# Kernel tuning notes

Measured on AMD Instinct MI355X. Metric: run time of the kernel, lower is better.

## Reference

```python
import jax, jax.numpy as jnp
import numpy as np

N = 50000       # nodes
E = 800000      # edges (before self loops)
F_IN = 256      # num_features
HID = 64        # hidden_dim
HEADS = 4       # num_heads
NEG = 0.2       # negative_slope
LN_EPS = 1e-5


def setup_inputs() -> dict:
    key = jax.random.key(0)
    ks = jax.random.split(key, 24)
    g = lambda k, shape, s=0.05: jax.random.normal(k, shape, jnp.float32) * s
    inp = {
        "x": jax.random.normal(ks[0], (N, F_IN), jnp.float32),
        "edge_index": jax.random.randint(ks[1], (2, E), 0, N, jnp.int32),
        # gat1: in=F_IN, out=HID per head, HEADS heads, concat=True
        "W1": g(ks[2], (HEADS * HID, F_IN)),
        "att_src1": g(ks[3], (HEADS, HID)),
        "att_dst1": g(ks[4], (HEADS, HID)),
        "b1": g(ks[5], (HEADS * HID,)),
        # gat2: in=HEADS*HID, out=HID, 1 head
        "W2": g(ks[6], (HID, HEADS * HID)),
        "att_src2": g(ks[7], (1, HID)),
        "att_dst2": g(ks[8], (1, HID)),
        "b2": g(ks[9], (HID,)),
        # lin_in residual projection
        "lin_w": g(ks[10], (HID, F_IN)),
        "lin_b": g(ks[11], (HID,)),
        # LayerNorm
        "gamma": jnp.ones((HID,), jnp.float32),
        "beta": jnp.zeros((HID,), jnp.float32),
        # GRU (1 layer, input=HID, hidden=HID), gate order r,z,n as in torch
        "w_ih": g(ks[12], (3 * HID, HID)),
        "w_hh": g(ks[13], (3 * HID, HID)),
        "b_ih": g(ks[14], (3 * HID,)),
        "b_hh": g(ks[15], (3 * HID,)),
        # fc head -> 3 classes
        "fc_w": g(ks[16], (3, HID)),
        "fc_b": g(ks[17], (3,)),
    }
    return inp


def gat_conv(x, W, att_src, att_dst, bias, src, dst, heads, n_nodes):
    """PyG-style GATConv (eval mode: no dropout). src/dst include self loops."""
    h = (x @ W.T).reshape(n_nodes, heads, -1)            # [N,H,C]
    a_src = jnp.einsum('nhc,hc->nh', h, att_src)          # [N,H]
    a_dst = jnp.einsum('nhc,hc->nh', h, att_dst)
    e = jax.nn.leaky_relu(a_src[src] + a_dst[dst], NEG)   # [E',H]
    m = jax.ops.segment_max(e, dst, num_segments=n_nodes) # scatter-softmax over dst
    e = jnp.exp(e - m[dst])
    s = jax.ops.segment_sum(e, dst, num_segments=n_nodes)
    alpha = e / s[dst]                                    # [E',H]
    out = jax.ops.segment_sum(alpha[:, :, None] * h[src], dst, num_segments=n_nodes)
    return out.reshape(n_nodes, -1) + bias                # concat heads + bias


def reference(x, edge_index, W1, att_src1, att_dst1, b1, W2, att_src2, att_dst2, b2,
              lin_w, lin_b, gamma, beta, w_ih, w_hh, b_ih, b_hh, fc_w, fc_b):
    n = x.shape[0]
    loops = jnp.arange(n, dtype=edge_index.dtype)
    src = jnp.concatenate([edge_index[0], loops])  # add_self_loops=True default
    dst = jnp.concatenate([edge_index[1], loops])

    h = jax.nn.leaky_relu(gat_conv(x, W1, att_src1, att_dst1, b1, src, dst, HEADS, n), NEG)
    # F.dropout is identity in eval mode
    h = gat_conv(h, W2, att_src2, att_dst2, b2, src, dst, 1, n)
    h = jax.nn.leaky_relu(h, NEG)
    # LayerNorm (torch uses biased variance)
    mu = h.mean(-1, keepdims=True)
    var = ((h - mu) ** 2).mean(-1, keepdims=True)
    h = (h - mu) / jnp.sqrt(var + LN_EPS) * gamma + beta
    h = h + x @ lin_w.T + lin_b
    # single-step GRU with h0 = 0 (seq_len == 1)
    gi = h @ w_ih.T + b_ih                 # [N,3C]
    i_r, i_z, i_n = jnp.split(gi, 3, axis=-1)
    h_r, h_z, h_n = jnp.split(b_hh, 3)     # W_hh @ 0 == 0
    r = jax.nn.sigmoid(i_r + h_r)
    z = jax.nn.sigmoid(i_z + h_z)
    ng = jnp.tanh(i_n + r * h_n)
    hy = (1.0 - z) * ng                    # + z * h_prev(=0)
    return hy @ fc_w.T + fc_b              # [N,3]
```

## Files before the change

kernel.cpp:

```cpp
#include <hip/hip_runtime.h>
#include <hip/hip_bf16.h>

#define N_NODES 50000
#define N_EDGES 800000
#define F_IN 256
#define HID 64
#define HEADS 4
#define NEG 0.2f
#define LN_EPS 1e-5f

typedef _Float16 half8 __attribute__((ext_vector_type(8)));
typedef _Float16 half4v __attribute__((ext_vector_type(4)));
typedef _Float16 half2v __attribute__((ext_vector_type(2)));
typedef float floatx4 __attribute__((ext_vector_type(4)));

union H2U { unsigned u; half2v h; };
union H8U { half8 v; half2v h2[4]; };

__device__ __forceinline__ float wave_sum(float v) {
    #pragma unroll
    for (int o = 32; o > 0; o >>= 1) v += __shfl_xor(v, o, 64);
    return v;
}
__device__ __forceinline__ float leaky(float x) { return x > 0.0f ? x : NEG * x; }

__device__ __forceinline__ half8 load_a8(const _Float16* p) { return *(const half8*)p; }
__device__ __forceinline__ half8 load_a8(const float* p) {
    float4 f0 = *(const float4*)p;
    float4 f1 = *(const float4*)(p + 4);
    half8 h;
    h[0] = (_Float16)f0.x; h[1] = (_Float16)f0.y;
    h[2] = (_Float16)f0.z; h[3] = (_Float16)f0.w;
    h[4] = (_Float16)f1.x; h[5] = (_Float16)f1.y;
    h[6] = (_Float16)f1.z; h[7] = (_Float16)f1.w;
    return h;
}

__global__ __launch_bounds__(256, 2)
void front_kernel(const float* __restrict__ x,
                  const float* __restrict__ W1, const float* __restrict__ lin_w,
                  const float* __restrict__ lin_b,
                  const float* __restrict__ att_s, const float* __restrict__ att_d,
                  _Float16* __restrict__ h1L, float* __restrict__ a_srcO,
                  float* __restrict__ a_dstO,
                  const int* __restrict__ src, const int* __restrict__ dst,
                  int* __restrict__ deg, int* __restrict__ colb,
                  const float* __restrict__ W2, const float* __restrict__ w_ih,
                  _Float16* __restrict__ W2h, _Float16* __restrict__ w_ihh,
                  int M, int E, int Etot, int GB, int SB) {
    if ((int)blockIdx.x >= GB) {
        int b2 = blockIdx.x - GB;
        if (b2 < SB) {
            int e = b2 * 256 + threadIdx.x;
            if (e >= Etot) return;
            int s, d;
            if (e < E) { s = src[e]; d = dst[e]; }
            else       { s = d = e - E; }
            int pos = atomicAdd(&deg[d], 1);
            if (pos < 64) colb[d * 64 + pos] = s;
        } else {
            int rel = ((b2 - SB) * 256 + threadIdx.x) * 4;
            const float* s; _Float16* dp;
            if      (rel < 16384) { s = W2; dp = W2h; }
            else if ((rel -= 16384) < 12288) { s = w_ih; dp = w_ihh; }
            else return;
            float4 v = *(const float4*)(s + rel);
            half4v h;
            h[0] = (_Float16)v.x; h[1] = (_Float16)v.y;
            h[2] = (_Float16)v.z; h[3] = (_Float16)v.w;
            *(half4v*)(dp + rel) = h;
        }
        return;
    }
    constexpr int NT = 20, Nc = 320, K = 256;
    constexpr int BROW = 40;
    constexpr int BTILE = Nc * BROW * 2;
    constexpr int NCS = 328;
    constexpr int TILE2B = 8 * NCS * 2;
    __shared__ __align__(16) char smem[BTILE];
    _Float16* sB = (_Float16*)smem;
    int tid = threadIdx.x;
    int w = tid >> 6, lane = tid & 63;
    int m_base = blockIdx.x * 64 + w * 16;
    bool active = (m_base < M);
    int r = lane & 15, q = lane >> 4;
    const float* ap = x + (size_t)(m_base + r) * K + q * 8;
    floatx4 acc[NT];
    #pragma unroll
    for (int t = 0; t < NT; ++t) acc[t] = (floatx4){0.f, 0.f, 0.f, 0.f};
    half8 a_next = {};
    if (active) a_next = load_a8(ap);
    for (int k0 = 0; k0 < K; k0 += 32) {
        for (int i = tid; i < Nc * 4; i += 256) {
            int row = i >> 2, seg = i & 3;
            const float* bp = (row < 256 ? W1 + (size_t)row * 256
                                         : lin_w + (size_t)(row - 256) * 256) + k0 + seg * 8;
            *(half8*)(sB + row * BROW + seg * 8) = load_a8(bp);
        }
        __syncthreads();
        half8 a = a_next;
        if (active && k0 + 32 < K) a_next = load_a8(ap + k0 + 32);
        if (active) {
            half8 b[NT];
            #pragma unroll
            for (int t = 0; t < NT; ++t)
                b[t] = *(const half8*)(sB + (t * 16 + r) * BROW + q * 8);
            #pragma unroll
            for (int t = 0; t < NT; ++t)
                acc[t] = __builtin_amdgcn_mfma_f32_16x16x32_f16(a, b[t], acc[t], 0, 0, 0);
        }
        __syncthreads();
    }
    if (active) {
        _Float16* st = (_Float16*)(smem + w * TILE2B);
        #pragma unroll
        for (int p = 0; p < 2; ++p) {
            #pragma unroll
            for (int t = 0; t < NT; ++t) {
                int cc = t * 16 + r;
                float bv = (cc >= 256) ? lin_b[cc - 256] : 0.f;
                #pragma unroll
                for (int rr2 = 0; rr2 < 2; ++rr2)
                    st[(q * 2 + rr2) * NCS + cc] = (_Float16)(acc[t][p * 2 + rr2] + bv);
            }
            #pragma unroll
            for (int it = 0; it < 5; ++it) {
                int idx = it * 64 + lane;
                int rowc = idx / 40, col = idx - rowc * 40;
                int grow = m_base + (rowc >> 1) * 4 + p * 2 + (rowc & 1);
                *((int4*)(h1L + (size_t)grow * 320) + col) =
                    *((const int4*)(st + rowc * NCS) + col);
            }
        }
        float ps[HEADS][4], pd[HEADS][4];
        #pragma unroll
        for (int h = 0; h < HEADS; ++h) {
            #pragma unroll
            for (int rr = 0; rr < 4; ++rr) { ps[h][rr] = 0.f; pd[h][rr] = 0.f; }
            #pragma unroll
            for (int tt = 0; tt < 4; ++tt) {
                int t = h * 4 + tt;
                float as = att_s[t * 16 + r];
                float ad = att_d[t * 16 + r];
                #pragma unroll
                for (int rr = 0; rr < 4; ++rr) {
                    ps[h][rr] += acc[t][rr] * as;
                    pd[h][rr] += acc[t][rr] * ad;
                }
            }
        }
        #pragma unroll
        for (int m = 1; m < 16; m <<= 1) {
            #pragma unroll
            for (int h = 0; h < HEADS; ++h)
                #pragma unroll
                for (int rr = 0; rr < 4; ++rr) {
                    ps[h][rr] += __shfl_xor(ps[h][rr], m, 64);
                    pd[h][rr] += __shfl_xor(pd[h][rr], m, 64);
                }
        }
        if (r == 0) {
            #pragma unroll
            for (int rr = 0; rr < 4; ++rr) {
                int gm = m_base + q * 4 + rr;
                #pragma unroll
                for (int h = 0; h < HEADS; ++h) {
                    a_srcO[gm * HEADS + h] = ps[h][rr];
                    a_dstO[gm * HEADS + h] = pd[h][rr];
                }
            }
        }
    }
}

template<int NT, int H, typename OutT, typename AT>
__global__ __launch_bounds__(256, 2)
void gemm_mfma(const AT* __restrict__ A, const _Float16* __restrict__ B,
               const float* __restrict__ bias, OutT* __restrict__ Cout,
               const float* __restrict__ att_s, const float* __restrict__ att_d,
               float* __restrict__ a_srcO, float* __restrict__ a_dstO,
               int M, int K, int bias_mode) {
    constexpr int Nc = NT * 16;
    constexpr int BROW = 40;
    constexpr int BTILE = Nc * BROW * 2;
    constexpr int TILEB = 16 * Nc * sizeof(OutT);
    constexpr int SM = (BTILE > 4 * TILEB) ? BTILE : 4 * TILEB;
    __shared__ __align__(16) char smem[SM];
    _Float16* sB = (_Float16*)smem;
    int tid = threadIdx.x;
    int w = tid >> 6, lane = tid & 63;
    int m_base = blockIdx.x * 64 + w * 16;
    bool active = (m_base < M);
    int r = lane & 15, q = lane >> 4;
    const AT* ap = A + (size_t)(m_base + r) * K + q * 8;
    floatx4 acc[NT];
    #pragma unroll
    for (int t = 0; t < NT; ++t) acc[t] = (floatx4){0.f, 0.f, 0.f, 0.f};
    half8 a_next = {};
    if (active) a_next = load_a8(ap);
    for (int k0 = 0; k0 < K; k0 += 32) {
        for (int i = tid; i < Nc * 4; i += 256) {
            int row = i >> 2, seg = i & 3;
            *(half8*)(sB + row * BROW + seg * 8) =
                *(const half8*)(B + (size_t)row * K + k0 + seg * 8);
        }
        __syncthreads();
        half8 a = a_next;
        if (active && k0 + 32 < K) a_next = load_a8(ap + k0 + 32);
        if (active) {
            half8 b[NT];
            #pragma unroll
            for (int t = 0; t < NT; ++t)
                b[t] = *(const half8*)(sB + (t * 16 + r) * BROW + q * 8);
            #pragma unroll
            for (int t = 0; t < NT; ++t)
                acc[t] = __builtin_amdgcn_mfma_f32_16x16x32_f16(a, b[t], acc[t], 0, 0, 0);
        }
        __syncthreads();
    }
    if (active) {
        OutT* st = (OutT*)(smem + w * TILEB);
        #pragma unroll
        for (int t = 0; t < NT; ++t) {
            int cc = t * 16 + r;
            float bv = 0.f;
            if (bias_mode == 1) bv = bias[cc];
            #pragma unroll
            for (int rr = 0; rr < 4; ++rr)
                st[(q * 4 + rr) * Nc + cc] = (OutT)(acc[t][rr] + bv);
        }
        constexpr int NISS = TILEB / 1024;
        const int4* src = (const int4*)st;
        int4* dst = (int4*)((char*)Cout + (size_t)m_base * (Nc * sizeof(OutT)));
        #pragma unroll
        for (int i = 0; i < NISS; ++i) dst[i * 64 + lane] = src[i * 64 + lane];
        if constexpr (H > 0) {
            float ps[H][4], pd[H][4];
            #pragma unroll
            for (int h = 0; h < H; ++h) {
                #pragma unroll
                for (int rr = 0; rr < 4; ++rr) { ps[h][rr] = 0.f; pd[h][rr] = 0.f; }
                #pragma unroll
                for (int tt = 0; tt < 4; ++tt) {
                    int t = h * 4 + tt;
                    float as = att_s[t * 16 + r];
                    float ad = att_d[t * 16 + r];
                    #pragma unroll
                    for (int rr = 0; rr < 4; ++rr) {
                        ps[h][rr] += acc[t][rr] * as;
                        pd[h][rr] += acc[t][rr] * ad;
                    }
                }
            }
            #pragma unroll
            for (int m = 1; m < 16; m <<= 1) {
                #pragma unroll
                for (int h = 0; h < H; ++h)
                    #pragma unroll
                    for (int rr = 0; rr < 4; ++rr) {
                        ps[h][rr] += __shfl_xor(ps[h][rr], m, 64);
                        pd[h][rr] += __shfl_xor(pd[h][rr], m, 64);
                    }
            }
            if (r == 0) {
                #pragma unroll
                for (int rr = 0; rr < 4; ++rr) {
                    int gm = m_base + q * 4 + rr;
                    #pragma unroll
                    for (int h = 0; h < H; ++h) {
                        a_srcO[gm * H + h] = ps[h][rr];
                        a_dstO[gm * H + h] = pd[h][rr];
                    }
                }
            }
        }
    }
}

__global__ void gat_agg4(const _Float16* __restrict__ h, const float* __restrict__ a_src,
                         const float* __restrict__ a_dst, const int* __restrict__ degA,
                         const int* __restrict__ colb, const float* __restrict__ bias,
                         _Float16* __restrict__ outp, int N) {
    int w = threadIdx.x >> 6, lane = threadIdx.x & 63;
    int i = blockIdx.x * 4 + w;
    if (i >= N) return;
    __shared__ unsigned alphS[4][256];
    __shared__ int      scolS[4][64];
    unsigned* alph = alphS[w];
    int*      scol = scolS[w];
    int deg = degA[i];
    deg = deg > 64 ? 64 : deg;
    float4 ad4 = *(const float4*)(a_dst + i * 4);

    float e0 = 0.f, e1 = 0.f, e2 = 0.f, e3 = 0.f; int s = 0;
    if (lane < deg) {
        s = colb[i * 64 + lane];
        float4 as4 = *(const float4*)(a_src + (size_t)s * 4);
        e0 = __expf(leaky(as4.x + ad4.x));
        e1 = __expf(leaky(as4.y + ad4.y));
        e2 = __expf(leaky(as4.z + ad4.z));
        e3 = __expf(leaky(as4.w + ad4.w));
    }
    float s0 = wave_sum(e0), s1 = wave_sum(e1), s2 = wave_sum(e2), s3 = wave_sum(e3);
    float4 al = make_float4(0.f, 0.f, 0.f, 0.f);
    int so = 0;
    if (lane < deg) {
        al = make_float4(e0 / s0, e1 / s1, e2 / s2, e3 / s3);
        so = s * 640;
    }
    H2U p0, p1, p2, p3;
    _Float16 t0 = (_Float16)al.x; p0.h = (half2v){t0, t0};
    _Float16 t1 = (_Float16)al.y; p1.h = (half2v){t1, t1};
    _Float16 t2 = (_Float16)al.z; p2.h = (half2v){t2, t2};
    _Float16 t3 = (_Float16)al.w; p3.h = (half2v){t3, t3};
    *(uint4*)(alph + lane * 4) = make_uint4(p0.u, p1.u, p2.u, p3.u);
    scol[lane] = so;
    int half32 = lane >> 5;
    int fl = lane & 31;
    int flb = fl * 16;
    int ahofs = half32 * 4 + (fl >> 3);
    const char* hB = (const char*)h;
    float acc[8];
    #pragma unroll
    for (int k = 0; k < 8; ++k) acc[k] = 0.f;
    int dpad = (deg + 7) & ~7;
    for (int j = 0; j < dpad; j += 8) {
        int o0 = scol[j + half32];
        int o1 = scol[j + 2 + half32];
        int o2 = scol[j + 4 + half32];
        int o3 = scol[j + 6 + half32];
        H8U v0, v1, v2, v3;
        v0.v = *(const half8*)(hB + (flb + o0));
        v1.v = *(const half8*)(hB + (flb + o1));
        v2.v = *(const half8*)(hB + (flb + o2));
        v3.v = *(const half8*)(hB + (flb + o3));
        H2U a0, a1, a2, a3;
        a0.u = alph[j * 4 + ahofs];
        a1.u = alph[j * 4 + 8 + ahofs];
        a2.u = alph[j * 4 + 16 + ahofs];
        a3.u = alph[j * 4 + 24 + ahofs];
        #pragma unroll
        for (int p = 0; p < 4; ++p) {
            half2v hp = a0.h * v0.h2[p];
            hp = __builtin_elementwise_fma(a1.h, v1.h2[p], hp);
            hp = __builtin_elementwise_fma(a2.h, v2.h2[p], hp);
            hp = __builtin_elementwise_fma(a3.h, v3.h2[p], hp);
            acc[p * 2]     += (float)hp[0];
            acc[p * 2 + 1] += (float)hp[1];
        }
    }
    #pragma unroll
    for (int k = 0; k < 8; ++k) acc[k] += __shfl_xor(acc[k], 32, 64);
    if (lane < 32) {
        half8 o8;
        #pragma unroll
        for (int k = 0; k < 8; ++k)
            o8[k] = (_Float16)leaky(acc[k] + bias[fl * 8 + k]);
        *(half8*)(outp + (size_t)i * 256 + fl * 8) = o8;
    }
}

__global__ void gat_agg1_ln(const _Float16* __restrict__ h, const float* __restrict__ a_src,
                            const float* __restrict__ a_dst, const int* __restrict__ degA,
                            const int* __restrict__ colb, const float* __restrict__ bias,
                            const _Float16* __restrict__ linh, const float* __restrict__ gamma,
                            const float* __restrict__ beta, _Float16* __restrict__ hresh,
                            int N) {
    int w = threadIdx.x >> 6, lane = threadIdx.x & 63;
    int i = blockIdx.x * 4 + w;
    if (i >= N) return;
    __shared__ unsigned alphS[4][80];
    __shared__ int      scolS[4][80];
    unsigned* alph = alphS[w];
    int*      scol = scolS[w];
    int deg = degA[i];
    deg = deg > 64 ? 64 : deg;
    float ad = a_dst[i];
    int f0 = (lane & 7) * 8;
    float acc[8];
    #pragma unroll
    for (int k = 0; k < 8; ++k) acc[k] = 0.f;

    float e = 0.f; int s = 0;
    if (lane < deg) {
        s = colb[i * 64 + lane];
        e = __expf(leaky(a_src[s] + ad));
    }
    float ss = wave_sum(e);
    H2U pa; pa.u = 0;
    int so = 0;
    if (lane < deg) {
        _Float16 ah = (_Float16)(e / ss);
        pa.h = (half2v){ah, ah};
        so = s << 7;
    }
    alph[lane] = pa.u;
    scol[lane] = so;
    if (lane < 16) { alph[64 + lane] = 0; scol[64 + lane] = 0; }
    int g = lane >> 3;
    int fb = (lane & 7) * 16;
    const char* hB = (const char*)h;
    int dpad = (deg + 15) & ~15;
    for (int j = 0; j < dpad; j += 16) {
        int o0 = scol[j + g];
        int o1 = scol[j + 8 + g];
        H8U v0, v1;
        v0.v = *(const half8*)(hB + (fb + o0));
        v1.v = *(const half8*)(hB + (fb + o1));
        H2U a0, a1;
        a0.u = alph[j + g];
        a1.u = alph[j + 8 + g];
        #pragma unroll
        for (int p = 0; p < 4; ++p) {
            half2v hp = a0.h * v0.h2[p];
            hp = __builtin_elementwise_fma(a1.h, v1.h2[p], hp);
            acc[p * 2]     += (float)hp[0];
            acc[p * 2 + 1] += (float)hp[1];
        }
    }
    #pragma unroll
    for (int k = 0; k < 8; ++k) {
        acc[k] += __shfl_xor(acc[k], 8, 64);
        acc[k] += __shfl_xor(acc[k], 16, 64);
        acc[k] += __shfl_xor(acc[k], 32, 64);
    }
    float4 b0 = *(const float4*)(bias + f0);
    float4 b1 = *(const float4*)(bias + f0 + 4);
    float o[8];
    o[0] = leaky(acc[0] + b0.x); o[1] = leaky(acc[1] + b0.y);
    o[2] = leaky(acc[2] + b0.z); o[3] = leaky(acc[3] + b0.w);
    o[4] = leaky(acc[4] + b1.x); o[5] = leaky(acc[5] + b1.y);
    o[6] = leaky(acc[6] + b1.z); o[7] = leaky(acc[7] + b1.w);
    float ls = 0.f;
    #pragma unroll
    for (int k = 0; k < 8; ++k) ls += o[k];
    ls += __shfl_xor(ls, 1, 64); ls += __shfl_xor(ls, 2, 64); ls += __shfl_xor(ls, 4, 64);
    float mu = ls * (1.0f / 64.0f);
    float lq = 0.f;
    #pragma unroll
    for (int k = 0; k < 8; ++k) { o[k] -= mu; lq += o[k] * o[k]; }
    lq += __shfl_xor(lq, 1, 64); lq += __shfl_xor(lq, 2, 64); lq += __shfl_xor(lq, 4, 64);
    float rstd = rsqrtf(lq * (1.0f / 64.0f) + LN_EPS);
    float4 g0 = *(const float4*)(gamma + f0);
    float4 g1 = *(const float4*)(gamma + f0 + 4);
    float4 be0 = *(const float4*)(beta + f0);
    float4 be1 = *(const float4*)(beta + f0 + 4);
    half8 l8 = *(const half8*)(linh + (size_t)i * 320 + f0);
    if (lane < 8) {
        half8 hv;
        hv[0] = (_Float16)(o[0] * rstd * g0.x + be0.x + (float)l8[0]);
        hv[1] = (_Float16)(o[1] * rstd * g0.y + be0.y + (float)l8[1]);
        hv[2] = (_Float16)(o[2] * rstd * g0.z + be0.z + (float)l8[2]);
        hv[3] = (_Float16)(o[3] * rstd * g0.w + be0.w + (float)l8[3]);
        hv[4] = (_Float16)(o[4] * rstd * g1.x + be1.x + (float)l8[4]);
        hv[5] = (_Float16)(o[5] * rstd * g1.y + be1.y + (float)l8[5]);
        hv[6] = (_Float16)(o[6] * rstd * g1.z + be1.z + (float)l8[6]);
        hv[7] = (_Float16)(o[7] * rstd * g1.w + be1.w + (float)l8[7]);
        *(half8*)(hresh + (size_t)i * 64 + f0) = hv;
    }
}

__global__ __launch_bounds__(256, 2)
void gemm_gru(const _Float16* __restrict__ A, const _Float16* __restrict__ B,
              const float* __restrict__ b_ih, const float* __restrict__ b_hh,
              const float* __restrict__ fc_w, const float* __restrict__ fc_b,
              float* __restrict__ outp, int M) {
    const int K = 64, NT = 12, Nc = 192;
    constexpr int BROW = 40;
    __shared__ __align__(16) char smem[4 * 16 * 192 * 2];
    _Float16* sB = (_Float16*)smem;
    int tid = threadIdx.x;
    int w = tid >> 6, lane = tid & 63;
    int m_base = blockIdx.x * 64 + w * 16;
    bool active = (m_base < M);
    int r = lane & 15, q = lane >> 4;
    const _Float16* ap = A + (size_t)(m_base + r) * K + q * 8;
    floatx4 acc[NT];
    #pragma unroll
    for (int t = 0; t < NT; ++t) acc[t] = (floatx4){0.f, 0.f, 0.f, 0.f};
    half8 a_next = {};
    if (active) a_next = *(const half8*)ap;
    for (int k0 = 0; k0 < K; k0 += 32) {
        for (int i = tid; i < Nc * 4; i += 256) {
            int row = i >> 2, seg = i & 3;
            *(half8*)(sB + row * BROW + seg * 8) =
                *(const half8*)(B + (size_t)row * K + k0 + seg * 8);
        }
        __syncthreads();
        half8 a = a_next;
        if (active && k0 + 32 < K) a_next = *(const half8*)(ap + k0 + 32);
        if (active) {
            half8 b[NT];
            #pragma unroll
            for (int t = 0; t < NT; ++t)
                b[t] = *(const half8*)(sB + (t * 16 + r) * BROW + q * 8);
            #pragma unroll
            for (int t = 0; t < NT; ++t)
                acc[t] = __builtin_amdgcn_mfma_f32_16x16x32_f16(a, b[t], acc[t], 0, 0, 0);
        }
        __syncthreads();
    }
    if (!active) return;
    _Float16* sw = (_Float16*)smem + w * 16 * 192;
    #pragma unroll
    for (int t = 0; t < NT; ++t) {
        int cc = t * 16 + r;
        float bv = b_ih[cc];
        #pragma unroll
        for (int rr = 0; rr < 4; ++rr)
            sw[(q * 4 + rr) * Nc + cc] = (_Float16)(acc[t][rr] + bv);
    }
    float br_[4], bz_[4], bn_[4], f0_[4], f1_[4], f2_[4];
    *(float4*)br_ = *(const float4*)(b_hh + r * 4);
    *(float4*)bz_ = *(const float4*)(b_hh + 64 + r * 4);
    *(float4*)bn_ = *(const float4*)(b_hh + 128 + r * 4);
    *(float4*)f0_ = *(const float4*)(fc_w + r * 4);
    *(float4*)f1_ = *(const float4*)(fc_w + 64 + r * 4);
    *(float4*)f2_ = *(const float4*)(fc_w + 128 + r * 4);
    #pragma unroll
    for (int rr = 0; rr < 4; ++rr) {
        int row = q * 4 + rr;
        const _Float16* g = sw + row * Nc;
        half4v ir4 = *(const half4v*)(g + r * 4);
        half4v iz4 = *(const half4v*)(g + 64 + r * 4);
        half4v in4 = *(const half4v*)(g + 128 + r * 4);
        float p0 = 0.f, p1 = 0.f, p2 = 0.f;
        #pragma unroll
        for (int k = 0; k < 4; ++k) {
            float rg = 1.0f / (1.0f + __expf(-((float)ir4[k] + br_[k])));
            float zg = 1.0f / (1.0f + __expf(-((float)iz4[k] + bz_[k])));
            float ng = tanhf((float)in4[k] + rg * bn_[k]);
            float hy = (1.0f - zg) * ng;
            p0 += hy * f0_[k]; p1 += hy * f1_[k]; p2 += hy * f2_[k];
        }
        #pragma unroll
        for (int o = 1; o <= 8; o <<= 1) {
            p0 += __shfl_xor(p0, o, 64);
            p1 += __shfl_xor(p1, o, 64);
            p2 += __shfl_xor(p2, o, 64);
        }
        if (r == 0) {
            int gm = m_base + row;
            outp[(size_t)gm * 3 + 0] = p0 + fc_b[0];
            outp[(size_t)gm * 3 + 1] = p1 + fc_b[1];
            outp[(size_t)gm * 3 + 2] = p2 + fc_b[2];
        }
    }
}

extern "C" void kernel_launch(void* const* d_in, const int* in_sizes, int n_in,
                              void* d_out, int out_size, void* d_ws, size_t ws_size,
                              hipStream_t stream) {
    const float* x        = (const float*)d_in[0];
    const int*   ei       = (const int*)d_in[1];
    const float* W1       = (const float*)d_in[2];
    const float* att_src1 = (const float*)d_in[3];
    const float* att_dst1 = (const float*)d_in[4];
    const float* b1       = (const float*)d_in[5];
    const float* W2       = (const float*)d_in[6];
    const float* att_src2 = (const float*)d_in[7];
    const float* att_dst2 = (const float*)d_in[8];
    const float* b2       = (const float*)d_in[9];
    const float* lin_w    = (const float*)d_in[10];
    const float* lin_b    = (const float*)d_in[11];
    const float* gamma    = (const float*)d_in[12];
    const float* beta     = (const float*)d_in[13];
    const float* w_ih     = (const float*)d_in[14];
    const float* b_ih     = (const float*)d_in[16];
    const float* b_hh     = (const float*)d_in[17];
    const float* fc_w     = (const float*)d_in[18];
    const float* fc_b     = (const float*)d_in[19];
    float* out = (float*)d_out;

    const int N = N_NODES, E = N_EDGES;
    const int Etot = E + N;
    char* ws = (char*)d_ws;

    size_t off = 0;
    auto alloc = [&](size_t bytes) {
        size_t o = off;
        off = (off + bytes + 255) & ~(size_t)255;
        return o;
    };
    int*      deg     = (int*)(ws + alloc((size_t)N * 4));
    int*      colb    = (int*)(ws + alloc((size_t)N * 64 * 4));
    float*    a_src1b = (float*)(ws + alloc((size_t)N * HEADS * 4));
    float*    a_dst1b = (float*)(ws + alloc((size_t)N * HEADS * 4));
    float*    a_src2b = (float*)(ws + alloc((size_t)N * 4));
    float*    a_dst2b = (float*)(ws + alloc((size_t)N * 4));
    _Float16* W2h     = (_Float16*)(ws + alloc((size_t)64 * 256 * 2));
    _Float16* w_ihh   = (_Float16*)(ws + alloc((size_t)192 * 64 * 2));
    _Float16* h1L  = (_Float16*)(ws + alloc((size_t)32000000));
    char* r3 = ws + alloc((size_t)25600000);
    _Float16* o1h   = (_Float16*)r3;
    _Float16* hresh = (_Float16*)r3;
    char* r4 = ws + alloc((size_t)6400000);
    _Float16* h2h = (_Float16*)r4;

    hipMemsetAsync(deg, 0, (size_t)N * 4, stream);

    const int gmBlocks = (N + 63) / 64;
    const int aggBlocks = (N + 3) / 4;
    const int SB = (Etot + 255) / 256;
    const int CB = ((16384 + 12288) / 4 + 255) / 256;

    front_kernel<<<gmBlocks + SB + CB, 256, 0, stream>>>(x, W1, lin_w, lin_b,
        att_src1, att_dst1, h1L, a_src1b, a_dst1b,
        ei, ei + E, deg, colb, W2, w_ih, W2h, w_ihh,
        N, E, Etot, gmBlocks, SB);

    gat_agg4<<<aggBlocks, 256, 0, stream>>>(h1L, a_src1b, a_dst1b, deg, colb, b1, o1h, N);

    gemm_mfma<4, 1, _Float16, _Float16><<<gmBlocks, 256, 0, stream>>>(o1h, W2h, nullptr, h2h,
        att_src2, att_dst2, a_src2b, a_dst2b, N, 256, 0);

    gat_agg1_ln<<<aggBlocks, 256, 0, stream>>>(h2h, a_src2b, a_dst2b, deg, colb, b2,
        h1L + 256, gamma, beta, hresh, N);

    gemm_gru<<<gmBlocks, 256, 0, stream>>>(hresh, w_ihh, b_ih, b_hh, fc_w, fc_b, out, N);
}
```

Measured before the change: 345.1 us.

## Interleave GEMM and edge-scatter blocks in front kernel; contiguous row-tile stores

Interleaves GEMM blocks with the edge-scatter and weight-conversion blocks in the front kernel (every fifth block does GEMM) so compute-heavy and atomic-heavy work share the GPU at the same time instead of running back to back. It also changes the epilogue so each half-wave writes 8 consecutive rows into an unpadded shared tile, letting the global store copy one contiguous 8x320 chunk. Dropping the padding can add LDS bank conflicts, and the new block mapping must keep every index in range.

```diff
diff --git a/kernel.cpp b/kernel.cpp
--- a/kernel.cpp
+++ b/kernel.cpp
@@ -48,8 +48,11 @@
                   const float* __restrict__ W2, const float* __restrict__ w_ih,
                   _Float16* __restrict__ W2h, _Float16* __restrict__ w_ihh,
                   int M, int E, int Etot, int GB, int SB) {
-    if ((int)blockIdx.x >= GB) {
-        int b2 = blockIdx.x - GB;
+    int bid = blockIdx.x;
+    bool is_gemm = (bid % 5 == 0) && (bid / 5 < GB);
+    if (!is_gemm) {
+        int ng = (bid >= 5 * GB) ? GB : (bid + 4) / 5;
+        int b2 = bid - ng;
         if (b2 < SB) {
             int e = b2 * 256 + threadIdx.x;
             if (e >= Etot) return;
@@ -72,16 +75,16 @@
         }
         return;
     }
+    int gblk = bid / 5;
     constexpr int NT = 20, Nc = 320, K = 256;
     constexpr int BROW = 40;
     constexpr int BTILE = Nc * BROW * 2;
-    constexpr int NCS = 328;
-    constexpr int TILE2B = 8 * NCS * 2;
+    constexpr int TILE2B = 8 * Nc * 2;
     __shared__ __align__(16) char smem[BTILE];
     _Float16* sB = (_Float16*)smem;
     int tid = threadIdx.x;
     int w = tid >> 6, lane = tid & 63;
-    int m_base = blockIdx.x * 64 + w * 16;
+    int m_base = gblk * 64 + w * 16;
     bool active = (m_base < M);
     int r = lane & 15, q = lane >> 4;
     const float* ap = x + (size_t)(m_base + r) * K + q * 8;
@@ -115,22 +118,21 @@
         _Float16* st = (_Float16*)(smem + w * TILE2B);
         #pragma unroll
         for (int p = 0; p < 2; ++p) {
-            #pragma unroll
-            for (int t = 0; t < NT; ++t) {
-                int cc = t * 16 + r;
-                float bv = (cc >= 256) ? lin_b[cc - 256] : 0.f;
-                #pragma unroll
-                for (int rr2 = 0; rr2 < 2; ++rr2)
-                    st[(q * 2 + rr2) * NCS + cc] = (_Float16)(acc[t][p * 2 + rr2] + bv);
+            if ((q >> 1) == p) {
+                #pragma unroll
+                for (int t = 0; t < NT; ++t) {
+                    int cc = t * 16 + r;
+                    float bv = (cc >= 256) ? lin_b[cc - 256] : 0.f;
+                    #pragma unroll
+                    for (int rr = 0; rr < 4; ++rr)
+                        st[((q & 1) * 4 + rr) * Nc + cc] = (_Float16)(acc[t][rr] + bv);
+                }
             }
-            #pragma unroll
-            for (int it = 0; it < 5; ++it) {
-                int idx = it * 64 + lane;
-                int rowc = idx / 40, col = idx - rowc * 40;
-                int grow = m_base + (rowc >> 1) * 4 + p * 2 + (rowc & 1);
-                *((int4*)(h1L + (size_t)grow * 320) + col) =
-                    *((const int4*)(st + rowc * NCS) + col);
-            }
+            const int4* srcp = (const int4*)st;
+            int4* dstp = (int4*)(h1L + (size_t)(m_base + p * 8) * Nc);
+            #pragma unroll
+            for (int it = 0; it < 5; ++it)
+                dstp[it * 64 + lane] = srcp[it * 64 + lane];
         }
         float ps[HEADS][4], pd[HEADS][4];
         #pragma unroll
@@ -603,8 +605,9 @@
     const int aggBlocks = (N + 3) / 4;
     const int SB = (Etot + 255) / 256;
     const int CB = ((16384 + 12288) / 4 + 255) / 256;
-
-    front_kernel<<<gmBlocks + SB + CB, 256, 0, stream>>>(x, W1, lin_w, lin_b,
+    const int FT = gmBlocks + SB + CB;
+
+    front_kernel<<<FT, 256, 0, stream>>>(x, W1, lin_w, lin_b,
         att_src1, att_dst1, h1L, a_src1b, a_dst1b,
         ei, ei + E, deg, colb, W2, w_ih, W2h, w_ihh,
         N, E, Etot, gmBlocks, SB);
```

Result: faster. 306.3 us (-11.2%).
